# Kernel tuning notes

Measured on AMD Instinct MI355X. Metric: run time of the kernel, lower is better.

The kernel has to match this reference:

```python
import jax, jax.numpy as jnp
import numpy as np

IN, H, FC1, FC2, OUT = 3, 30, 64, 32, 1
B, T = 8192, 256


def _lstm_layer(xT, W_ih, W_hh, b_ih, b_hh):
    """xT: (T, B, Din). Returns (hidden sequence (T,B,H), final h (B,H)).
    PyTorch gate order: i, f, g, o."""
    # Precompute input contribution for all timesteps (one big GEMM).
    gx = jnp.einsum('tbd,gd->tbg', xT, W_ih) + b_ih + b_hh  # (T,B,4H)
    b = xT.shape[1]
    h0 = jnp.zeros((b, W_hh.shape[1]), xT.dtype)
    c0 = h0

    def step(carry, g):
        h, c = carry
        gates = g + h @ W_hh.T
        i, f, gg, o = jnp.split(gates, 4, axis=-1)
        i = jax.nn.sigmoid(i)
        f = jax.nn.sigmoid(f)
        gg = jnp.tanh(gg)
        o = jax.nn.sigmoid(o)
        c = f * c + i * gg
        h = o * jnp.tanh(c)
        return (h, c), h

    (h_n, _), ys = jax.lax.scan(step, (h0, c0), gx)
    return ys, h_n


def setup_inputs() -> dict:
    key = jax.random.key(0)
    ks = jax.random.split(key, 16)
    s = 0.18  # ~1/sqrt(hidden_size), matches PyTorch uniform init scale
    inp = {
        'x': jax.random.normal(ks[0], (B, T, IN), jnp.float32),
        'W_ih0': jax.random.normal(ks[1], (4 * H, IN), jnp.float32) * s,
        'W_hh0': jax.random.normal(ks[2], (4 * H, H), jnp.float32) * s,
        'b_ih0': jax.random.normal(ks[3], (4 * H,), jnp.float32) * s,
        'b_hh0': jax.random.normal(ks[4], (4 * H,), jnp.float32) * s,
        'W_ih1': jax.random.normal(ks[5], (4 * H, H), jnp.float32) * s,
        'W_hh1': jax.random.normal(ks[6], (4 * H, H), jnp.float32) * s,
        'b_ih1': jax.random.normal(ks[7], (4 * H,), jnp.float32) * s,
        'b_hh1': jax.random.normal(ks[8], (4 * H,), jnp.float32) * s,
        'W_fc1': jax.random.normal(ks[9], (FC1, H), jnp.float32) * s,
        'b_fc1': jax.random.normal(ks[10], (FC1,), jnp.float32) * s,
        'W_fc2': jax.random.normal(ks[11], (FC2, FC1), jnp.float32) * 0.125,
        'b_fc2': jax.random.normal(ks[12], (FC2,), jnp.float32) * 0.125,
        'W_fc3': jax.random.normal(ks[13], (OUT, FC2), jnp.float32) * 0.17,
        'b_fc3': jax.random.normal(ks[14], (OUT,), jnp.float32) * 0.17,
    }
    return inp


def reference(x, W_ih0, W_hh0, b_ih0, b_hh0, W_ih1, W_hh1, b_ih1, b_hh1,
              W_fc1, b_fc1, W_fc2, b_fc2, W_fc3, b_fc3):
    xT = jnp.swapaxes(x, 0, 1)  # (T,B,IN)
    ys, _ = _lstm_layer(xT, W_ih0, W_hh0, b_ih0, b_hh0)   # layer 0 sequence
    _, h_n = _lstm_layer(ys, W_ih1, W_hh1, b_ih1, b_hh1)  # layer 1 final h
    # FC head (dropout = identity in eval mode)
    z = jax.nn.relu(h_n @ W_fc1.T + b_fc1)
    z = jax.nn.relu(z @ W_fc2.T + b_fc2)
    z = jax.nn.sigmoid(z @ W_fc3.T + b_fc3)
    return z.squeeze(-1)  # (B,)
```

## Files before the change

kernel.cpp:

```cpp
#include <hip/hip_runtime.h>

#define TT   256
#define HID  30
#define LOG2E 1.4426950408889634f
#define HS   40
#define NR   16

typedef __bf16 bf16x8_t __attribute__((ext_vector_type(8)));
typedef float  f32x4_t  __attribute__((ext_vector_type(4)));
typedef unsigned int u32x4_t __attribute__((ext_vector_type(4)));

__device__ __forceinline__ float fexp2(float x){
#if __has_builtin(__builtin_amdgcn_exp2f)
    return __builtin_amdgcn_exp2f(x);
#else
    return exp2f(x);
#endif
}
__device__ __forceinline__ float frcp(float x){
#if __has_builtin(__builtin_amdgcn_rcpf)
    return __builtin_amdgcn_rcpf(x);
#else
    return 1.f/x;
#endif
}
__device__ __forceinline__ float fsigmoid(float x){ return frcp(1.f + fexp2(-LOG2E*x)); }
__device__ __forceinline__ f32x4_t exp4(f32x4_t v){
    f32x4_t e; e[0]=fexp2(v[0]); e[1]=fexp2(v[1]); e[2]=fexp2(v[2]); e[3]=fexp2(v[3]); return e;
}
__device__ __forceinline__ f32x4_t rcp4(f32x4_t v){
    f32x4_t r; r[0]=frcp(v[0]); r[1]=frcp(v[1]); r[2]=frcp(v[2]); r[3]=frcp(v[3]); return r;
}

__device__ __forceinline__ uint32_t pk_bf16(float lo, float hi){
    uint32_t r;
    asm("v_cvt_pk_bf16_f32 %0, %1, %2" : "=v"(r) : "v"(lo), "v"(hi));
    return r;
}

__device__ __forceinline__ int ld_acq(int* p){
    return __hip_atomic_load(p, __ATOMIC_ACQUIRE, __HIP_MEMORY_SCOPE_WORKGROUP);
}
__device__ __forceinline__ void st_rel(int* p, int v){
    __hip_atomic_store(p, v, __ATOMIC_RELEASE, __HIP_MEMORY_SCOPE_WORKGROUP);
}

__device__ __forceinline__ f32x4_t lstm_act(f32x4_t aI, f32x4_t aF, f32x4_t aG,
                                            f32x4_t aO, f32x4_t& cst){
    f32x4_t eI = exp4(aI);
    f32x4_t eF = exp4(aF);
    f32x4_t eG = exp4(aG);
    f32x4_t eO = exp4(aO);
    f32x4_t D1 = eF + 1.f;
    f32x4_t tG = eG + 1.f;
    f32x4_t D2 = eI*tG + tG;
    f32x4_t r  = rcp4(D1*D2);
    f32x4_t f  = r*D2;
    f32x4_t p  = (eG - 1.f) * (r*D1);
    cst = f*cst + p;
    f32x4_t cc;
    cc[0]=fminf(fmaxf(cst[0],-30.f),30.f);
    cc[1]=fminf(fmaxf(cst[1],-30.f),30.f);
    cc[2]=fminf(fmaxf(cst[2],-30.f),30.f);
    cc[3]=fminf(fmaxf(cst[3],-30.f),30.f);
    f32x4_t eC = exp4(cc * (2.f*LOG2E));
    f32x4_t tC = eC + 1.f;
    f32x4_t dn = eO*tC + tC;
    return (eC - 1.f) * rcp4(dn);
}

__global__ __launch_bounds__(128, 1)
void lstm_fused(const float* __restrict__ x,
    const float* __restrict__ Wih0, const float* __restrict__ Whh0,
    const float* __restrict__ bih0, const float* __restrict__ bhh0,
    const float* __restrict__ Wih1, const float* __restrict__ Whh1,
    const float* __restrict__ bih1, const float* __restrict__ bhh1,
    const float* __restrict__ Wfc1, const float* __restrict__ bfc1,
    const float* __restrict__ Wfc2, const float* __restrict__ bfc2,
    const float* __restrict__ Wfc3, const float* __restrict__ bfc3,
    float* __restrict__ out)
{
    __shared__ __align__(16) __bf16 ring[NR][16][HS];
    __shared__ __align__(4)  __bf16 xlds01[TT+1][16][2];
    __shared__ __align__(16) float  xlds2[TT][16];
    __shared__ float h1_last[16][32];
    __shared__ float zbuf[16][64];
    __shared__ float z2buf[16][32];
    __shared__ int   flags[2];

    const int tid  = threadIdx.x;
    const int lane = tid & 63;
    const int wv   = tid >> 6;
    const int n    = lane & 15;
    const int q    = lane >> 4;
    const int q4   = q*4;
    const int bbase = blockIdx.x * 16;

    {
        const float* xg = x + (size_t)bbase*(TT*3);
        for (int i4 = tid*4; i4 < 16*TT*3; i4 += 128*4) {
            int row = i4 / (TT*3), tc0 = i4 % (TT*3);
            f32x4_t v = *(const f32x4_t*)(xg + (size_t)row*(TT*3) + tc0);
            #pragma unroll
            for (int j = 0; j < 4; ++j) {
                int tc = tc0 + j;
                int t = tc/3, c = tc - 3*t;
                if (c == 2) xlds2[t][row] = v[j];
                else        xlds01[t][row][c] = (__bf16)v[j];
            }
        }
        if (tid < 32) xlds01[TT][tid>>1][tid&1] = (__bf16)0.f;
        if (tid == 0) { flags[0]=0; flags[1]=0; }
    }

    const int  ad01 = 4*(n + 32*(q & 1));
    const int  ad23 = ad01 + 64;
    const bool qlo  = (q < 2);
    const bool q3   = (q == 3);

    __syncthreads();

#define MF(A,B,C) __builtin_amdgcn_mfma_f32_16x16x32_bf16((A),(B),(C),0,0,0)
#define BP(a,s)   ((uint32_t)__builtin_amdgcn_ds_bpermute((a),(int)(s)))
#define XPOSE(hA, hB, XW, dst) do {                                            \
    uint32_t a01=pk_bf16((hA)[0],(hA)[1]), a23=pk_bf16((hA)[2],(hA)[3]);       \
    uint32_t b01=pk_bf16((hB)[0],(hB)[1]), b23=pk_bf16((hB)[2],(hB)[3]);       \
    uint32_t t0a=BP(ad01,a01), t1a=BP(ad01,a23), t2a=BP(ad23,a01), t3a=BP(ad23,a23); \
    uint32_t t0b=BP(ad01,b01), t1b=BP(ad01,b23), t2b=BP(ad23,b01), t3b=BP(ad23,b23); \
    u32x4_t fw;                                                                \
    fw[0] = qlo ? t0a : t0b;                                                   \
    fw[1] = qlo ? t1a : t1b;                                                   \
    fw[2] = qlo ? t2a : t2b;                                                   \
    fw[3] = q3 ? (XW) : (qlo ? t3a : t3b);                                     \
    (dst) = __builtin_bit_cast(bf16x8_t, fw);                                  \
} while (0)

    const float scl[4] = {-LOG2E, -LOG2E, 2.f*LOG2E, -LOG2E};

    if (wv == 0) {
        bf16x8_t w0[4][2];
        f32x4_t  bq0[4][2], wxq[4][2];
        #pragma unroll
        for (int g = 0; g < 4; ++g) {
            #pragma unroll
            for (int ch = 0; ch < 2; ++ch) {
                const float sg = scl[g];
                const int uf = ch*16 + n;
                const int uqf = (uf < HID) ? uf : 0;
                const int rowf = g*HID + uqf;
                bf16x8_t a{};
                #pragma unroll
                for (int j = 0; j < 8; ++j) {
                    const int k = q*8 + j;
                    float va;
                    if (k < HID)       va = Whh0[rowf*HID + k];
                    else if (k == 30)  va = Wih0[rowf*3 + 0];
                    else               va = Wih0[rowf*3 + 1];
                    a[j] = (__bf16)(sg*va);
                }
                w0[g][ch] = a;
                f32x4_t b0v, wxv;
                #pragma unroll
                for (int r = 0; r < 4; ++r) {
                    const int ub = ch*16 + q4 + r;
                    const int uqb = (ub < HID) ? ub : 0;
                    const int rowb = g*HID + uqb;
                    b0v[r] = sg*(bih0[rowb] + bhh0[rowb]);
                    wxv[r] = sg*Wih0[rowb*3 + 2];
                }
                bq0[g][ch] = b0v;  wxq[g][ch] = wxv;
            }
        }

        bf16x8_t h0frag;
        {
            u32x4_t z = {0u,0u,0u,0u};
            if (q3) z[3] = *(const uint32_t*)&xlds01[0][n][0];
            h0frag = __builtin_bit_cast(bf16x8_t, z);
        }
        f32x4_t c0A = {0,0,0,0}, c0B = {0,0,0,0};
        int consv = 0;

        #pragma unroll 1
        for (int s = 0; s < TT; ++s) {
            if (s - consv > NR-4) {
                do { consv = ld_acq(&flags[1]); } while (s - consv > NR-1);
            }
            const float x2v = xlds2[s][n];
            f32x4_t aI0 = MF(w0[0][0], h0frag, bq0[0][0] + wxq[0][0]*x2v);
            f32x4_t aF0 = MF(w0[1][0], h0frag, bq0[1][0] + wxq[1][0]*x2v);
            f32x4_t aG0 = MF(w0[2][0], h0frag, bq0[2][0] + wxq[2][0]*x2v);
            f32x4_t aO0 = MF(w0[3][0], h0frag, bq0[3][0] + wxq[3][0]*x2v);
            f32x4_t aI1 = MF(w0[0][1], h0frag, bq0[0][1] + wxq[0][1]*x2v);
            f32x4_t aF1 = MF(w0[1][1], h0frag, bq0[1][1] + wxq[1][1]*x2v);
            f32x4_t aG1 = MF(w0[2][1], h0frag, bq0[2][1] + wxq[2][1]*x2v);
            f32x4_t aO1 = MF(w0[3][1], h0frag, bq0[3][1] + wxq[3][1]*x2v);
            f32x4_t h0A = lstm_act(aI0, aF0, aG0, aO0, c0A);
            f32x4_t h0B = lstm_act(aI1, aF1, aG1, aO1, c0B);
            const uint32_t XW = *(const uint32_t*)&xlds01[s+1][n][0];
            XPOSE(h0A, h0B, XW, h0frag);
            *(bf16x8_t*)&ring[s & (NR-1)][n][q*8] = h0frag;
            if (lane == 0) st_rel(&flags[0], s+1);
        }
    } else {
        bf16x8_t wi1[4][2], wh1[4][2];
        f32x4_t  bq1[4][2];
        #pragma unroll
        for (int g = 0; g < 4; ++g) {
            #pragma unroll
            for (int ch = 0; ch < 2; ++ch) {
                const float sg = scl[g];
                const int uf = ch*16 + n;
                const int uqf = (uf < HID) ? uf : 0;
                const int rowf = g*HID + uqf;
                bf16x8_t a{}, b{};
                #pragma unroll
                for (int j = 0; j < 8; ++j) {
                    const int k = q*8 + j;
                    float va = 0.f, vb = 0.f;
                    if (k < HID) { va = Wih1[rowf*HID + k];  vb = Whh1[rowf*HID + k]; }
                    a[j] = (__bf16)(sg*va);
                    b[j] = (__bf16)(sg*vb);
                }
                wi1[g][ch] = a;  wh1[g][ch] = b;
                f32x4_t b1v;
                #pragma unroll
                for (int r = 0; r < 4; ++r) {
                    const int ub = ch*16 + q4 + r;
                    const int uqb = (ub < HID) ? ub : 0;
                    const int rowb = g*HID + uqb;
                    b1v[r] = sg*(bih1[rowb] + bhh1[rowb]);
                }
                bq1[g][ch] = b1v;
            }
        }

        bf16x8_t h1frag;
        { u32x4_t z = {0u,0u,0u,0u}; h1frag = __builtin_bit_cast(bf16x8_t, z); }
        f32x4_t c1A = {0,0,0,0}, c1B = {0,0,0,0};
        int seqv = 0;

        #pragma unroll 1
        for (int s = 0; s < TT; ++s) {
            if (seqv < s+1) {
                do { seqv = ld_acq(&flags[0]); } while (seqv < s+1);
            }
            __builtin_amdgcn_sched_barrier(0);
            bf16x8_t A1 = *(const bf16x8_t*)&ring[s & (NR-1)][n][q*8];
            f32x4_t dI0 = MF(wi1[0][0], A1, bq1[0][0]);
            f32x4_t dF0 = MF(wi1[1][0], A1, bq1[1][0]);
            f32x4_t dG0 = MF(wi1[2][0], A1, bq1[2][0]);
            f32x4_t dO0 = MF(wi1[3][0], A1, bq1[3][0]);
            f32x4_t dI1 = MF(wi1[0][1], A1, bq1[0][1]);
            f32x4_t dF1 = MF(wi1[1][1], A1, bq1[1][1]);
            f32x4_t dG1 = MF(wi1[2][1], A1, bq1[2][1]);
            f32x4_t dO1 = MF(wi1[3][1], A1, bq1[3][1]);
            dI0 = MF(wh1[0][0], h1frag, dI0);
            dF0 = MF(wh1[1][0], h1frag, dF0);
            dG0 = MF(wh1[2][0], h1frag, dG0);
            dO0 = MF(wh1[3][0], h1frag, dO0);
            dI1 = MF(wh1[0][1], h1frag, dI1);
            dF1 = MF(wh1[1][1], h1frag, dF1);
            dG1 = MF(wh1[2][1], h1frag, dG1);
            dO1 = MF(wh1[3][1], h1frag, dO1);
            f32x4_t h1A = lstm_act(dI0, dF0, dG0, dO0, c1A);
            f32x4_t h1B = lstm_act(dI1, dF1, dG1, dO1, c1B);
            if (s == TT-1) {
                *(f32x4_t*)&h1_last[n][q4]    = h1A;
                *(f32x4_t*)&h1_last[n][16+q4] = h1B;
            } else {
                XPOSE(h1A, h1B, 0u, h1frag);
            }
            if (((s & 3) == 3) && lane == 0) st_rel(&flags[1], s+1);
        }
    }
#undef XPOSE
#undef BP
#undef MF

    __syncthreads();

    #pragma unroll
    for (int rep = 0; rep < 8; ++rep) {
        int idx = tid + rep*128;
        int m = idx >> 6, uu = idx & 63;
        float a = bfc1[uu];
        for (int k = 0; k < HID; ++k) a += h1_last[m][k] * Wfc1[uu*HID+k];
        zbuf[m][uu] = fmaxf(a, 0.f);
    }
    __syncthreads();
    #pragma unroll
    for (int rep = 0; rep < 4; ++rep) {
        int idx = tid + rep*128;
        int m = idx >> 5, v = idx & 31;
        float a = bfc2[v];
        for (int k = 0; k < 64; ++k) a += zbuf[m][k] * Wfc2[v*64+k];
        z2buf[m][v] = fmaxf(a, 0.f);
    }
    __syncthreads();
    if (tid < 16) {
        float a = bfc3[0];
        for (int k = 0; k < 32; ++k) a += z2buf[tid][k] * Wfc3[k];
        out[bbase + tid] = fsigmoid(a);
    }
}

extern "C" void kernel_launch(void* const* d_in, const int* in_sizes, int n_in,
                              void* d_out, int out_size, void* d_ws, size_t ws_size,
                              hipStream_t stream) {
    const float* x    = (const float*)d_in[0];
    const float* Wih0 = (const float*)d_in[1];
    const float* Whh0 = (const float*)d_in[2];
    const float* bih0 = (const float*)d_in[3];
    const float* bhh0 = (const float*)d_in[4];
    const float* Wih1 = (const float*)d_in[5];
    const float* Whh1 = (const float*)d_in[6];
    const float* bih1 = (const float*)d_in[7];
    const float* bhh1 = (const float*)d_in[8];
    const float* Wfc1 = (const float*)d_in[9];
    const float* bfc1 = (const float*)d_in[10];
    const float* Wfc2 = (const float*)d_in[11];
    const float* bfc2 = (const float*)d_in[12];
    const float* Wfc3 = (const float*)d_in[13];
    const float* bfc3 = (const float*)d_in[14];
    float* outp = (float*)d_out;

    hipLaunchKernelGGL(lstm_fused, dim3(512), dim3(128), 0, stream,
        x, Wih0, Whh0, bih0, bhh0, Wih1, Whh1, bih1, bhh1,
        Wfc1, bfc1, Wfc2, bfc2, Wfc3, bfc3, outp);
}
```

Measured before the change: 307.8 us.

## Replace LDS flag spin-waits with chunked double-buffered barrier pipeline between layers

Wave 0 (layer 0) and wave 1 (layer 1) previously handed off per-timestep hidden states through an LDS ring guarded by acquire/release flag polling. Now they run in lockstep chunks of 8 timesteps with a __syncthreads after each chunk: layer 0 fills one half of a double buffer while layer 1 consumes the other half, one chunk behind. This removes the per-step atomic polling and lets the inner chunk loop unroll, at the cost of rigid barrier coupling. Any imbalance between the two waves within a chunk now stalls the faster one, and the pipeline gains one extra chunk of fill latency.

New measurement: 285.6 us. 1.08x faster.

```diff
diff --git a/kernel.cpp b/kernel.cpp
--- a/kernel.cpp
+++ b/kernel.cpp
@@ -1,10 +1,11 @@
 #include <hip/hip_runtime.h>
 
-#define TT   256
-#define HID  30
+#define TT    256
+#define HID   30
 #define LOG2E 1.4426950408889634f
-#define HS   40
-#define NR   16
+#define HS    40
+#define NR    16
+#define CHUNK 8
 
 typedef __bf16 bf16x8_t __attribute__((ext_vector_type(8)));
 typedef float  f32x4_t  __attribute__((ext_vector_type(4)));
@@ -36,13 +37,6 @@
     uint32_t r;
     asm("v_cvt_pk_bf16_f32 %0, %1, %2" : "=v"(r) : "v"(lo), "v"(hi));
     return r;
-}
-
-__device__ __forceinline__ int ld_acq(int* p){
-    return __hip_atomic_load(p, __ATOMIC_ACQUIRE, __HIP_MEMORY_SCOPE_WORKGROUP);
-}
-__device__ __forceinline__ void st_rel(int* p, int v){
-    __hip_atomic_store(p, v, __ATOMIC_RELEASE, __HIP_MEMORY_SCOPE_WORKGROUP);
 }
 
 __device__ __forceinline__ f32x4_t lstm_act(f32x4_t aI, f32x4_t aF, f32x4_t aG,
@@ -86,7 +80,6 @@
     __shared__ float h1_last[16][32];
     __shared__ float zbuf[16][64];
     __shared__ float z2buf[16][32];
-    __shared__ int   flags[2];
 
     const int tid  = threadIdx.x;
     const int lane = tid & 63;
@@ -110,7 +103,6 @@
             }
         }
         if (tid < 32) xlds01[TT][tid>>1][tid&1] = (__bf16)0.f;
-        if (tid == 0) { flags[0]=0; flags[1]=0; }
     }
 
     const int  ad01 = 4*(n + 32*(q & 1));
@@ -179,28 +171,32 @@
             h0frag = __builtin_bit_cast(bf16x8_t, z);
         }
         f32x4_t c0A = {0,0,0,0}, c0B = {0,0,0,0};
-        int consv = 0;
 
         #pragma unroll 1
-        for (int s = 0; s < TT; ++s) {
-            if (s - consv > NR-4) {
-                do { consv = ld_acq(&flags[1]); } while (s - consv > NR-1);
-            }
-            const float x2v = xlds2[s][n];
-            f32x4_t aI0 = MF(w0[0][0], h0frag, bq0[0][0] + wxq[0][0]*x2v);
-            f32x4_t aF0 = MF(w0[1][0], h0frag, bq0[1][0] + wxq[1][0]*x2v);
-            f32x4_t aG0 = MF(w0[2][0], h0frag, bq0[2][0] + wxq[2][0]*x2v);
-            f32x4_t aO0 = MF(w0[3][0], h0frag, bq0[3][0] + wxq[3][0]*x2v);
-            f32x4_t aI1 = MF(w0[0][1], h0frag, bq0[0][1] + wxq[0][1]*x2v);
-            f32x4_t aF1 = MF(w0[1][1], h0frag, bq0[1][1] + wxq[1][1]*x2v);
-            f32x4_t aG1 = MF(w0[2][1], h0frag, bq0[2][1] + wxq[2][1]*x2v);
-            f32x4_t aO1 = MF(w0[3][1], h0frag, bq0[3][1] + wxq[3][1]*x2v);
-            f32x4_t h0A = lstm_act(aI0, aF0, aG0, aO0, c0A);
-            f32x4_t h0B = lstm_act(aI1, aF1, aG1, aO1, c0B);
-            const uint32_t XW = *(const uint32_t*)&xlds01[s+1][n][0];
-            XPOSE(h0A, h0B, XW, h0frag);
-            *(bf16x8_t*)&ring[s & (NR-1)][n][q*8] = h0frag;
-            if (lane == 0) st_rel(&flags[0], s+1);
+        for (int c = 0; c <= TT/CHUNK; ++c) {
+            if (c < TT/CHUNK) {
+                const int sb   = c*CHUNK;
+                const int half = (c & 1)*CHUNK;
+                #pragma unroll
+                for (int j = 0; j < CHUNK; ++j) {
+                    const int s = sb + j;
+                    const float x2v = xlds2[s][n];
+                    f32x4_t aI0 = MF(w0[0][0], h0frag, bq0[0][0] + wxq[0][0]*x2v);
+                    f32x4_t aF0 = MF(w0[1][0], h0frag, bq0[1][0] + wxq[1][0]*x2v);
+                    f32x4_t aG0 = MF(w0[2][0], h0frag, bq0[2][0] + wxq[2][0]*x2v);
+                    f32x4_t aO0 = MF(w0[3][0], h0frag, bq0[3][0] + wxq[3][0]*x2v);
+                    f32x4_t aI1 = MF(w0[0][1], h0frag, bq0[0][1] + wxq[0][1]*x2v);
+                    f32x4_t aF1 = MF(w0[1][1], h0frag, bq0[1][1] + wxq[1][1]*x2v);
+                    f32x4_t aG1 = MF(w0[2][1], h0frag, bq0[2][1] + wxq[2][1]*x2v);
+                    f32x4_t aO1 = MF(w0[3][1], h0frag, bq0[3][1] + wxq[3][1]*x2v);
+                    f32x4_t h0A = lstm_act(aI0, aF0, aG0, aO0, c0A);
+                    f32x4_t h0B = lstm_act(aI1, aF1, aG1, aO1, c0B);
+                    const uint32_t XW = *(const uint32_t*)&xlds01[s+1][n][0];
+                    XPOSE(h0A, h0B, XW, h0frag);
+                    *(bf16x8_t*)&ring[half + j][n][q*8] = h0frag;
+                }
+            }
+            __syncthreads();
         }
     } else {
         bf16x8_t wi1[4][2], wh1[4][2];
@@ -238,47 +234,49 @@
         bf16x8_t h1frag;
         { u32x4_t z = {0u,0u,0u,0u}; h1frag = __builtin_bit_cast(bf16x8_t, z); }
         f32x4_t c1A = {0,0,0,0}, c1B = {0,0,0,0};
-        int seqv = 0;
 
         #pragma unroll 1
-        for (int s = 0; s < TT; ++s) {
-            if (seqv < s+1) {
-                do { seqv = ld_acq(&flags[0]); } while (seqv < s+1);
-            }
-            __builtin_amdgcn_sched_barrier(0);
-            bf16x8_t A1 = *(const bf16x8_t*)&ring[s & (NR-1)][n][q*8];
-            f32x4_t dI0 = MF(wi1[0][0], A1, bq1[0][0]);
-            f32x4_t dF0 = MF(wi1[1][0], A1, bq1[1][0]);
-            f32x4_t dG0 = MF(wi1[2][0], A1, bq1[2][0]);
-            f32x4_t dO0 = MF(wi1[3][0], A1, bq1[3][0]);
-            f32x4_t dI1 = MF(wi1[0][1], A1, bq1[0][1]);
-            f32x4_t dF1 = MF(wi1[1][1], A1, bq1[1][1]);
-            f32x4_t dG1 = MF(wi1[2][1], A1, bq1[2][1]);
-            f32x4_t dO1 = MF(wi1[3][1], A1, bq1[3][1]);
-            dI0 = MF(wh1[0][0], h1frag, dI0);
-            dF0 = MF(wh1[1][0], h1frag, dF0);
-            dG0 = MF(wh1[2][0], h1frag, dG0);
-            dO0 = MF(wh1[3][0], h1frag, dO0);
-            dI1 = MF(wh1[0][1], h1frag, dI1);
-            dF1 = MF(wh1[1][1], h1frag, dF1);
-            dG1 = MF(wh1[2][1], h1frag, dG1);
-            dO1 = MF(wh1[3][1], h1frag, dO1);
-            f32x4_t h1A = lstm_act(dI0, dF0, dG0, dO0, c1A);
-            f32x4_t h1B = lstm_act(dI1, dF1, dG1, dO1, c1B);
-            if (s == TT-1) {
-                *(f32x4_t*)&h1_last[n][q4]    = h1A;
-                *(f32x4_t*)&h1_last[n][16+q4] = h1B;
-            } else {
-                XPOSE(h1A, h1B, 0u, h1frag);
-            }
-            if (((s & 3) == 3) && lane == 0) st_rel(&flags[1], s+1);
+        for (int c = 0; c <= TT/CHUNK; ++c) {
+            if (c > 0) {
+                const int cc   = c - 1;
+                const int sb   = cc*CHUNK;
+                const int half = (cc & 1)*CHUNK;
+                #pragma unroll
+                for (int j = 0; j < CHUNK; ++j) {
+                    const int s = sb + j;
+                    bf16x8_t A1 = *(const bf16x8_t*)&ring[half + j][n][q*8];
+                    f32x4_t dI0 = MF(wi1[0][0], A1, bq1[0][0]);
+                    f32x4_t dF0 = MF(wi1[1][0], A1, bq1[1][0]);
+                    f32x4_t dG0 = MF(wi1[2][0], A1, bq1[2][0]);
+                    f32x4_t dO0 = MF(wi1[3][0], A1, bq1[3][0]);
+                    f32x4_t dI1 = MF(wi1[0][1], A1, bq1[0][1]);
+                    f32x4_t dF1 = MF(wi1[1][1], A1, bq1[1][1]);
+                    f32x4_t dG1 = MF(wi1[2][1], A1, bq1[2][1]);
+                    f32x4_t dO1 = MF(wi1[3][1], A1, bq1[3][1]);
+                    dI0 = MF(wh1[0][0], h1frag, dI0);
+                    dF0 = MF(wh1[1][0], h1frag, dF0);
+                    dG0 = MF(wh1[2][0], h1frag, dG0);
+                    dO0 = MF(wh1[3][0], h1frag, dO0);
+                    dI1 = MF(wh1[0][1], h1frag, dI1);
+                    dF1 = MF(wh1[1][1], h1frag, dF1);
+                    dG1 = MF(wh1[2][1], h1frag, dG1);
+                    dO1 = MF(wh1[3][1], h1frag, dO1);
+                    f32x4_t h1A = lstm_act(dI0, dF0, dG0, dO0, c1A);
+                    f32x4_t h1B = lstm_act(dI1, dF1, dG1, dO1, c1B);
+                    if (s == TT-1) {
+                        *(f32x4_t*)&h1_last[n][q4]    = h1A;
+                        *(f32x4_t*)&h1_last[n][16+q4] = h1B;
+                    } else {
+                        XPOSE(h1A, h1B, 0u, h1frag);
+                    }
+                }
+            }
+            __syncthreads();
         }
     }
 #undef XPOSE
 #undef BP
 #undef MF
-
-    __syncthreads();
 
     #pragma unroll
     for (int rep = 0; rep < 8; ++rep) {
```
